# Kernel optimization log

Hardware: AMD Instinct MI355X
Metric: run time of the kernel (lower is better)

Reference implementation:

```python
import jax, jax.numpy as jnp
import numpy as np

N_HEAD = 16
ROPE_BASE = 10000.0


def rope_cos_sin(T, head_dim, dtype):
    inv_freq = 1.0 / (ROPE_BASE ** (jnp.arange(0, head_dim, 2, dtype=jnp.float32) / head_dim))
    t = jnp.arange(T, dtype=jnp.float32)
    freqs = jnp.einsum('i,j->ij', t, inv_freq)          # [T, head_dim/2]
    emb = jnp.concatenate([freqs, freqs], axis=-1)       # [T, head_dim]
    return jnp.cos(emb).astype(dtype), jnp.sin(emb).astype(dtype)


def rotate_half(x):
    h = x.shape[-1] // 2
    return jnp.concatenate([-x[..., h:], x[..., :h]], axis=-1)


def setup_inputs() -> dict:
    key = jax.random.key(0)
    ks = jax.random.split(key, 5)
    B, T, C = 2, 1024, 2048
    s = 0.02
    return {
        'x': jax.random.normal(ks[0], (B, T, C), dtype=jnp.float32),
        'Wq': jax.random.normal(ks[1], (C, C), dtype=jnp.float32) * s,
        'Wk': jax.random.normal(ks[2], (C, C), dtype=jnp.float32) * s,
        'Wv': jax.random.normal(ks[3], (C, C), dtype=jnp.float32) * s,
        'Wo': jax.random.normal(ks[4], (C, C), dtype=jnp.float32) * s,
    }


def reference(x, Wq, Wk, Wv, Wo):
    B, T, C = x.shape
    H = N_HEAD
    D = C // H
    # torch Linear: y = x @ W.T  (W is [out, in])
    q = jnp.einsum('btc,oc->bto', x, Wq).reshape(B, T, H, D).transpose(0, 2, 1, 3)
    k = jnp.einsum('btc,oc->bto', x, Wk).reshape(B, T, H, D).transpose(0, 2, 1, 3)
    v = jnp.einsum('btc,oc->bto', x, Wv).reshape(B, T, H, D).transpose(0, 2, 1, 3)
    cos, sin = rope_cos_sin(T, D, x.dtype)               # [T, D]
    cos = cos[None, None]                                 # [1,1,T,D]
    sin = sin[None, None]
    q = q * cos + rotate_half(q) * sin
    k = k * cos + rotate_half(k) * sin
    scale = 1.0 / jnp.sqrt(jnp.asarray(D, dtype=x.dtype))
    att = jnp.einsum('bhqd,bhkd->bhqk', q, k) * scale    # [B,H,T,T]
    causal = jnp.tril(jnp.ones((T, T), dtype=bool))
    att = jnp.where(causal[None, None], att, jnp.finfo(x.dtype).min)
    att = jax.nn.softmax(att, axis=-1)
    y = jnp.einsum('bhqk,bhkd->bhqd', att, v)            # [B,H,T,D]
    y = y.transpose(0, 2, 1, 3).reshape(B, T, C)
    return jnp.einsum('btc,oc->bto', y, Wo)
```

## Files before the change

kernel.cpp:

```cpp
#include <hip/hip_runtime.h>
#include <stdint.h>

typedef unsigned short u16;
typedef __bf16 bf16x8 __attribute__((ext_vector_type(8)));
typedef float  f32x4  __attribute__((ext_vector_type(4)));

#define B_  2
#define T_  1024
#define C_  2048
#define H_  16
#define D_  128
#define NTENS 4194304

__device__ __forceinline__ u16 f2bf(float f) {
    union { float f; uint32_t u; } v; v.f = f;
    uint32_t r = (v.u + 0x7FFFu + ((v.u >> 16) & 1u)) >> 16;
    return (u16)r;
}
__device__ __forceinline__ float bf2f(u16 h) {
    union { uint32_t u; float f; } v; v.u = ((uint32_t)h) << 16;
    return v.f;
}

__global__ __launch_bounds__(256) void k_convert(
    const float* __restrict__ x, const float* __restrict__ wq,
    const float* __restrict__ wk, const float* __restrict__ wv,
    const float* __restrict__ wo, u16* __restrict__ dst)
{
    int z = blockIdx.z;
    const float* src = (z == 0) ? x : (z == 1) ? wq : (z == 2) ? wk : (z == 3) ? wv : wo;
    u16* d = dst + (size_t)z * NTENS;
    size_t i = ((size_t)blockIdx.x * 256 + threadIdx.x) * 4;
    float4 v = *(const float4*)(src + i);
    ushort4 o;
    o.x = f2bf(v.x); o.y = f2bf(v.y); o.z = f2bf(v.z); o.w = f2bf(v.w);
    *(ushort4*)(d + i) = o;
}

__global__ void k_rope_table(float* __restrict__ ct, float* __restrict__ st)
{
    int t = blockIdx.x, d = threadIdx.x;
    float inv = expf(-(float)d * (9.210340371976184f / 64.0f));
    float th = (float)t * inv;
    float s, c;
    sincosf(th, &s, &c);
    ct[t * 64 + d] = c;
    st[t * 64 + d] = s;
}

template<int MTILE, int EPI>
__device__ __forceinline__ void gemm_tile_nt(
    const u16* __restrict__ A, int lda,
    const u16* __restrict__ Bp, int ldb,
    void* __restrict__ Cp, int ldc,
    int m0, int n0, int K,
    u16* SMEM, const float* __restrict__ ct, const float* __restrict__ st, int z)
{
    constexpr int MF  = MTILE / 16;
    constexpr int ACH = MTILE / 32;
    u16* As = SMEM;
    u16* Bs = SMEM + MTILE * 64;

    const int tid  = threadIdx.x;
    const int wave = tid >> 6;
    const int lane = tid & 63;
    const int wc   = wave << 5;
    const int frow = lane & 15;
    const int quad = lane >> 4;

    const int lrow8  = lane >> 3;
    const int slot   = lane & 7;
    const int gchunk = slot ^ lrow8;

    f32x4 acc[MF][2] = {};

    size_t aoff[ACH], boff[4];
#pragma unroll
    for (int i = 0; i < ACH; ++i) {
        int c = (i << 2) + wave;
        int r = (c << 3) + lrow8;
        aoff[i] = (size_t)(m0 + r) * lda + (gchunk << 3);
    }
#pragma unroll
    for (int i = 0; i < 4; ++i) {
        int r = (i << 5) + (wave << 3) + lrow8;
        boff[i] = (size_t)(n0 + r) * ldb + (gchunk << 3);
    }

    for (int kt = 0; kt < K; kt += 64) {
#pragma unroll
        for (int i = 0; i < ACH; ++i) {
            int c = (i << 2) + wave;
            __builtin_amdgcn_global_load_lds(
                (const __attribute__((address_space(1))) void*)(A + aoff[i] + kt),
                (__attribute__((address_space(3))) void*)(As + (c << 9)), 16, 0, 0);
        }
#pragma unroll
        for (int i = 0; i < 4; ++i) {
            int c = (i << 2) + wave;
            __builtin_amdgcn_global_load_lds(
                (const __attribute__((address_space(1))) void*)(Bp + boff[i] + kt),
                (__attribute__((address_space(3))) void*)(Bs + (c << 9)), 16, 0, 0);
        }
        __syncthreads();

#pragma unroll
        for (int ks = 0; ks < 2; ++ks) {
            int lk = (ks << 2) + quad;
            bf16x8 af[MF], bfv[2];
#pragma unroll
            for (int i = 0; i < MF; ++i) {
                int ar = (i << 4) + frow;
                af[i] = *(const bf16x8*)&As[ar * 64 + ((lk ^ (frow & 7)) << 3)];
            }
#pragma unroll
            for (int j = 0; j < 2; ++j) {
                int br = wc + (j << 4) + frow;
                bfv[j] = *(const bf16x8*)&Bs[br * 64 + ((lk ^ (frow & 7)) << 3)];
            }
#pragma unroll
            for (int i = 0; i < MF; ++i)
#pragma unroll
                for (int j = 0; j < 2; ++j)
                    acc[i][j] = __builtin_amdgcn_mfma_f32_16x16x32_bf16(
                        af[i], bfv[j], acc[i][j], 0, 0, 0);
        }
        __syncthreads();
    }

    if constexpr (EPI == 2) {
        if (z < 2) {
            u16* L = SMEM;
#pragma unroll
            for (int i = 0; i < MF; ++i)
#pragma unroll
                for (int j = 0; j < 2; ++j)
#pragma unroll
                    for (int r = 0; r < 4; ++r) {
                        int rl = (i << 4) + (quad << 2) + r;
                        int d  = wc + (j << 4) + frow;
                        L[rl * 136 + d] = f2bf(acc[i][j][r]);
                    }
            __syncthreads();

            int rl = tid >> 2;
            int d0 = (tid & 3) << 4;
            int t  = (m0 + rl) & 1023;
            uint4 lo4[2], hi4[2];
            lo4[0] = *(const uint4*)&L[rl * 136 + d0];
            lo4[1] = *(const uint4*)&L[rl * 136 + d0 + 8];
            hi4[0] = *(const uint4*)&L[rl * 136 + 64 + d0];
            hi4[1] = *(const uint4*)&L[rl * 136 + 64 + d0 + 8];
            const u16* lo = (const u16*)lo4;
            const u16* hi = (const u16*)hi4;
            float sc = (z == 0) ? 0.08838834764831845f : 1.0f;
            u16 o0[16], o1[16];
            const float* ctp = ct + t * 64 + d0;
            const float* stp = st + t * 64 + d0;
#pragma unroll
            for (int e = 0; e < 16; ++e) {
                float c = ctp[e], s = stp[e];
                float a = bf2f(lo[e]), b = bf2f(hi[e]);
                o0[e] = f2bf((a * c - b * s) * sc);
                o1[e] = f2bf((b * c + a * s) * sc);
            }
            u16* Op = (u16*)Cp;
            size_t rbase = (size_t)(m0 + rl) * ldc + n0;
            *(uint4*)&Op[rbase + d0]          = ((uint4*)o0)[0];
            *(uint4*)&Op[rbase + d0 + 8]      = ((uint4*)o0)[1];
            *(uint4*)&Op[rbase + 64 + d0]     = ((uint4*)o1)[0];
            *(uint4*)&Op[rbase + 64 + d0 + 8] = ((uint4*)o1)[1];
            return;
        }
        u16* Op = (u16*)Cp;
#pragma unroll
        for (int i = 0; i < MF; ++i)
#pragma unroll
            for (int j = 0; j < 2; ++j)
#pragma unroll
                for (int r = 0; r < 4; ++r) {
                    int m = m0 + (i << 4) + (quad << 2) + r;
                    int n = n0 + wc + (j << 4) + frow;
                    Op[(size_t)m * ldc + n] = f2bf(acc[i][j][r]);
                }
        return;
    }

#pragma unroll
    for (int i = 0; i < MF; ++i)
#pragma unroll
        for (int j = 0; j < 2; ++j)
#pragma unroll
            for (int r = 0; r < 4; ++r) {
                int m = m0 + (i << 4) + (quad << 2) + r;
                int n = n0 + wc + (j << 4) + frow;
                if constexpr (EPI == 1)
                    ((u16*)Cp)[(size_t)m * ldc + n] = f2bf(acc[i][j][r]);
                else
                    ((float*)Cp)[(size_t)m * ldc + n] = acc[i][j][r];
            }
}

__global__ __launch_bounds__(256) void k_gemm_qkv(
    const u16* __restrict__ xb, const u16* __restrict__ wq,
    const u16* __restrict__ wk, const u16* __restrict__ wv,
    u16* __restrict__ q, u16* __restrict__ k, u16* __restrict__ v,
    const float* __restrict__ ct, const float* __restrict__ st)
{
    __shared__ u16 SMEM[64 * 64 + 128 * 64];
    int z = blockIdx.z;
    const u16* Bp = (z == 0) ? wq : (z == 1) ? wk : wv;
    u16* Op       = (z == 0) ? q  : (z == 1) ? k  : v;
    gemm_tile_nt<64, 2>(xb, C_, Bp, C_, Op, C_,
                        blockIdx.y * 64, blockIdx.x * 128, C_, SMEM, ct, st, z);
}

__global__ __launch_bounds__(256) void k_flash(
    const u16* __restrict__ qb, const u16* __restrict__ kb,
    const u16* __restrict__ vb, u16* __restrict__ yb)
{
    __shared__ u16 Qs[64 * 128];
    __shared__ u16 Ks[64 * 128];
    __shared__ u16 Vs[128 * 72];

    const int bx  = blockIdx.x;
    const int bh  = bx & 31, b = bh >> 4, h = bh & 15;
    const int qt  = (bx < 256) ? (15 - (bx >> 5)) : ((bx >> 5) - 8);
    const int tid = threadIdx.x, wave = tid >> 6, lane = tid & 63;
    const int frow = lane & 15, quad = lane >> 4;

    const u16* qbase = qb + (size_t)b * (T_ * C_) + h * D_;
    const u16* kbase = kb + (size_t)b * (T_ * C_) + h * D_;
    const u16* vbase = vb + (size_t)b * (T_ * C_) + h * D_;
    const int q0 = qt << 6;

    {
        const int r4 = lane >> 4, s16 = lane & 15;
#pragma unroll
        for (int i = 0; i < 4; ++i) {
            int c = (i << 2) + wave;
            int row = (c << 2) + r4;
            int g = (s16 & 8) | ((s16 & 7) ^ (row & 7));
            __builtin_amdgcn_global_load_lds(
                (const __attribute__((address_space(1))) void*)(qbase + (size_t)(q0 + row) * C_ + (g << 3)),
                (__attribute__((address_space(3))) void*)(Qs + (c << 9)), 16, 0, 0);
        }
    }

    f32x4 Y[8] = {};
    float mrow[4], lrow[4];
#pragma unroll
    for (int r = 0; r < 4; ++r) { mrow[r] = -3e38f; lrow[r] = 0.f; }

    const int tok = q0 + wave * 16 + quad * 4;

    for (int kt = 0; kt <= qt; ++kt) {
        const int k0 = kt << 6;
        {
            const int r4 = lane >> 4, s16 = lane & 15;
#pragma unroll
            for (int i = 0; i < 4; ++i) {
                int c = (i << 2) + wave;
                int row = (c << 2) + r4;
                int g = (s16 & 8) | ((s16 & 7) ^ (row & 7));
                __builtin_amdgcn_global_load_lds(
                    (const __attribute__((address_space(1))) void*)(kbase + (size_t)(k0 + row) * C_ + (g << 3)),
                    (__attribute__((address_space(3))) void*)(Ks + (c << 9)), 16, 0, 0);
            }
        }
        {
#pragma unroll
            for (int i = 0; i < 4; ++i) {
                int idx = (i << 8) + tid;
                int kr = idx & 63;
                int n8 = (idx >> 6) << 3;
                uint4 vv = *(const uint4*)&vbase[(size_t)(k0 + kr) * C_ + n8];
                u16 tmp[8];
                *(uint4*)tmp = vv;
#pragma unroll
                for (int e = 0; e < 8; ++e)
                    Vs[(n8 + e) * 72 + kr] = tmp[e];
            }
        }
        __syncthreads();

        f32x4 S[4] = {};
#pragma unroll
        for (int ks = 0; ks < 4; ++ks) {
            int lk = (ks << 2) + quad;
            int sw = ((lk & 8) | ((lk & 7) ^ (frow & 7))) << 3;
            bf16x8 a = *(const bf16x8*)&Qs[(wave * 16 + frow) * 128 + sw];
#pragma unroll
            for (int jj = 0; jj < 4; ++jj) {
                bf16x8 bb = *(const bf16x8*)&Ks[((jj << 4) + frow) * 128 + sw];
                S[jj] = __builtin_amdgcn_mfma_f32_16x16x32_bf16(a, bb, S[jj], 0, 0, 0);
            }
        }

        if (kt == qt) {
#pragma unroll
            for (int jj = 0; jj < 4; ++jj) {
                int colg = k0 + (jj << 4) + frow;
#pragma unroll
                for (int r = 0; r < 4; ++r)
                    if (colg > tok + r) S[jj][r] = -1e30f;
            }
        }

        float al[4];
#pragma unroll
        for (int r = 0; r < 4; ++r) {
            float tm = fmaxf(fmaxf(S[0][r], S[1][r]), fmaxf(S[2][r], S[3][r]));
#pragma unroll
            for (int off = 8; off > 0; off >>= 1) tm = fmaxf(tm, __shfl_xor(tm, off));
            float mn = fmaxf(mrow[r], tm);
            al[r] = __expf(mrow[r] - mn);
            mrow[r] = mn;
            float rs = 0.f;
#pragma unroll
            for (int jj = 0; jj < 4; ++jj) {
                float e = __expf(S[jj][r] - mn);
                S[jj][r] = e;
                rs += e;
            }
#pragma unroll
            for (int off = 8; off > 0; off >>= 1) rs += __shfl_xor(rs, off);
            lrow[r] = lrow[r] * al[r] + rs;
        }
#pragma unroll
        for (int dj = 0; dj < 8; ++dj)
#pragma unroll
            for (int r = 0; r < 4; ++r) Y[dj][r] *= al[r];

        __syncthreads();

        u16* Ps = Ks;
#pragma unroll
        for (int jj = 0; jj < 4; ++jj)
#pragma unroll
            for (int r = 0; r < 4; ++r)
                Ps[(wave * 16 + quad * 4 + r) * 72 + (jj << 4) + frow] = f2bf(S[jj][r]);

#pragma unroll
        for (int ks = 0; ks < 2; ++ks) {
            bf16x8 pa = *(const bf16x8*)&Ps[(wave * 16 + frow) * 72 + (ks << 5) + (quad << 3)];
#pragma unroll
            for (int dj = 0; dj < 8; ++dj) {
                bf16x8 vv = *(const bf16x8*)&Vs[((dj << 4) + frow) * 72 + (ks << 5) + (quad << 3)];
                Y[dj] = __builtin_amdgcn_mfma_f32_16x16x32_bf16(pa, vv, Y[dj], 0, 0, 0);
            }
        }
        __syncthreads();
    }

    u16* ybase = yb + (size_t)b * (T_ * C_) + h * D_;
#pragma unroll
    for (int r = 0; r < 4; ++r) {
        float inv = 1.0f / lrow[r];
#pragma unroll
        for (int dj = 0; dj < 8; ++dj)
            ybase[(size_t)(tok + r) * C_ + (dj << 4) + frow] = f2bf(Y[dj][r] * inv);
    }
}

__global__ __launch_bounds__(256) void k_gemm_out(
    const u16* __restrict__ yb, const u16* __restrict__ wo, float* __restrict__ out)
{
    __shared__ u16 SMEM[32 * 64 + 128 * 64];
    gemm_tile_nt<32, 0>(yb, C_, wo, C_, out, C_,
                        blockIdx.y * 32, blockIdx.x * 128, C_, SMEM, nullptr, nullptr, 0);
}

extern "C" void kernel_launch(void* const* d_in, const int* in_sizes, int n_in,
                              void* d_out, int out_size, void* d_ws, size_t ws_size,
                              hipStream_t stream)
{
    (void)in_sizes; (void)n_in; (void)out_size; (void)ws_size;
    const float* x  = (const float*)d_in[0];
    const float* Wq = (const float*)d_in[1];
    const float* Wk = (const float*)d_in[2];
    const float* Wv = (const float*)d_in[3];
    const float* Wo = (const float*)d_in[4];

    u16* ws  = (u16*)d_ws;
    u16* xb  = ws;
    u16* wqb = ws + (size_t)1 * NTENS;
    u16* wkb = ws + (size_t)2 * NTENS;
    u16* wvb = ws + (size_t)3 * NTENS;
    u16* wob = ws + (size_t)4 * NTENS;
    u16* qb  = ws + (size_t)5 * NTENS;
    u16* kb  = ws + (size_t)6 * NTENS;
    u16* vb  = ws + (size_t)7 * NTENS;
    u16* yb  = ws + (size_t)8 * NTENS;
    float* ct = (float*)(ws + (size_t)9 * NTENS);
    float* st = ct + 65536;

    k_convert   <<<dim3(4096, 1, 5), 256, 0, stream>>>(x, Wq, Wk, Wv, Wo, ws);
    k_rope_table<<<dim3(1024), 64, 0, stream>>>(ct, st);
    k_gemm_qkv  <<<dim3(16, 32, 3), 256, 0, stream>>>(xb, wqb, wkb, wvb, qb, kb, vb, ct, st);
    k_flash     <<<dim3(512), 256, 0, stream>>>(qb, kb, vb, yb);
    k_gemm_out  <<<dim3(16, 64, 1), 256, 0, stream>>>(yb, wob, (float*)d_out);
}
```

Baseline: 271.3 us.

## Remap GEMM wave columns for register RoPE, widen flash key tile, keep Q in registers

The GEMM wave-to-column mapping changes so each wave holds both halves of a head dimension, letting the RoPE epilogue run in registers without an LDS round trip and barrier. The flash kernel loads Q fragments straight into registers, doubles the key/value tile to 128 rows with a swizzled V layout, and so runs half as many outer iterations. The output GEMM moves to 64-row tiles with half the blocks. These cut LDS traffic, syncs and loop overhead, at the cost of more causal-mask waste on the diagonal tile, more LDS per flash block (lower occupancy), and scattered 2-byte stores in the RoPE epilogue.

New measurement: 262.9 us. 1.03x faster.

```diff
diff --git a/kernel.cpp b/kernel.cpp
--- a/kernel.cpp
+++ b/kernel.cpp
@@ -64,7 +64,6 @@
     const int tid  = threadIdx.x;
     const int wave = tid >> 6;
     const int lane = tid & 63;
-    const int wc   = wave << 5;
     const int frow = lane & 15;
     const int quad = lane >> 4;
 
@@ -115,7 +114,7 @@
             }
 #pragma unroll
             for (int j = 0; j < 2; ++j) {
-                int br = wc + (j << 4) + frow;
+                int br = (wave << 4) + (j << 6) + frow;
                 bfv[j] = *(const bf16x8*)&Bs[br * 64 + ((lk ^ (frow & 7)) << 3)];
             }
 #pragma unroll
@@ -130,60 +129,22 @@
 
     if constexpr (EPI == 2) {
         if (z < 2) {
-            u16* L = SMEM;
+            const int d = (wave << 4) + frow;
+            const float sc = (z == 0) ? 0.08838834764831845f : 1.0f;
+            u16* Op = (u16*)Cp;
 #pragma unroll
             for (int i = 0; i < MF; ++i)
-#pragma unroll
-                for (int j = 0; j < 2; ++j)
-#pragma unroll
-                    for (int r = 0; r < 4; ++r) {
-                        int rl = (i << 4) + (quad << 2) + r;
-                        int d  = wc + (j << 4) + frow;
-                        L[rl * 136 + d] = f2bf(acc[i][j][r]);
-                    }
-            __syncthreads();
-
-            int rl = tid >> 2;
-            int d0 = (tid & 3) << 4;
-            int t  = (m0 + rl) & 1023;
-            uint4 lo4[2], hi4[2];
-            lo4[0] = *(const uint4*)&L[rl * 136 + d0];
-            lo4[1] = *(const uint4*)&L[rl * 136 + d0 + 8];
-            hi4[0] = *(const uint4*)&L[rl * 136 + 64 + d0];
-            hi4[1] = *(const uint4*)&L[rl * 136 + 64 + d0 + 8];
-            const u16* lo = (const u16*)lo4;
-            const u16* hi = (const u16*)hi4;
-            float sc = (z == 0) ? 0.08838834764831845f : 1.0f;
-            u16 o0[16], o1[16];
-            const float* ctp = ct + t * 64 + d0;
-            const float* stp = st + t * 64 + d0;
-#pragma unroll
-            for (int e = 0; e < 16; ++e) {
-                float c = ctp[e], s = stp[e];
-                float a = bf2f(lo[e]), b = bf2f(hi[e]);
-                o0[e] = f2bf((a * c - b * s) * sc);
-                o1[e] = f2bf((b * c + a * s) * sc);
-            }
-            u16* Op = (u16*)Cp;
-            size_t rbase = (size_t)(m0 + rl) * ldc + n0;
-            *(uint4*)&Op[rbase + d0]          = ((uint4*)o0)[0];
-            *(uint4*)&Op[rbase + d0 + 8]      = ((uint4*)o0)[1];
-            *(uint4*)&Op[rbase + 64 + d0]     = ((uint4*)o1)[0];
-            *(uint4*)&Op[rbase + 64 + d0 + 8] = ((uint4*)o1)[1];
-            return;
-        }
-        u16* Op = (u16*)Cp;
-#pragma unroll
-        for (int i = 0; i < MF; ++i)
-#pragma unroll
-            for (int j = 0; j < 2; ++j)
 #pragma unroll
                 for (int r = 0; r < 4; ++r) {
                     int m = m0 + (i << 4) + (quad << 2) + r;
-                    int n = n0 + wc + (j << 4) + frow;
-                    Op[(size_t)m * ldc + n] = f2bf(acc[i][j][r]);
+                    int t = m & 1023;
+                    float c = ct[t * 64 + d], s = st[t * 64 + d];
+                    float a = acc[i][0][r], bb = acc[i][1][r];
+                    Op[(size_t)m * ldc + n0 + d]      = f2bf((a * c - bb * s) * sc);
+                    Op[(size_t)m * ldc + n0 + d + 64] = f2bf((bb * c + a * s) * sc);
                 }
-        return;
+            return;
+        }
     }
 
 #pragma unroll
@@ -193,11 +154,11 @@
 #pragma unroll
             for (int r = 0; r < 4; ++r) {
                 int m = m0 + (i << 4) + (quad << 2) + r;
-                int n = n0 + wc + (j << 4) + frow;
-                if constexpr (EPI == 1)
+                int n = n0 + (wave << 4) + (j << 6) + frow;
+                if constexpr (EPI == 0)
+                    ((float*)Cp)[(size_t)m * ldc + n] = acc[i][j][r];
+                else
                     ((u16*)Cp)[(size_t)m * ldc + n] = f2bf(acc[i][j][r]);
-                else
-                    ((float*)Cp)[(size_t)m * ldc + n] = acc[i][j][r];
             }
 }
 
@@ -219,13 +180,13 @@
     const u16* __restrict__ qb, const u16* __restrict__ kb,
     const u16* __restrict__ vb, u16* __restrict__ yb)
 {
-    __shared__ u16 Qs[64 * 128];
-    __shared__ u16 Ks[64 * 128];
-    __shared__ u16 Vs[128 * 72];
+    __shared__ u16 Ks[128 * 128];
+    __shared__ u16 Vs[128 * 128];
 
     const int bx  = blockIdx.x;
     const int bh  = bx & 31, b = bh >> 4, h = bh & 15;
     const int qt  = (bx < 256) ? (15 - (bx >> 5)) : ((bx >> 5) - 8);
+    const int KT  = (qt >> 1) + 1;
     const int tid = threadIdx.x, wave = tid >> 6, lane = tid & 63;
     const int frow = lane & 15, quad = lane >> 4;
 
@@ -234,32 +195,25 @@
     const u16* vbase = vb + (size_t)b * (T_ * C_) + h * D_;
     const int q0 = qt << 6;
 
-    {
-        const int r4 = lane >> 4, s16 = lane & 15;
-#pragma unroll
-        for (int i = 0; i < 4; ++i) {
-            int c = (i << 2) + wave;
-            int row = (c << 2) + r4;
-            int g = (s16 & 8) | ((s16 & 7) ^ (row & 7));
-            __builtin_amdgcn_global_load_lds(
-                (const __attribute__((address_space(1))) void*)(qbase + (size_t)(q0 + row) * C_ + (g << 3)),
-                (__attribute__((address_space(3))) void*)(Qs + (c << 9)), 16, 0, 0);
-        }
-    }
+    bf16x8 qf[4];
+#pragma unroll
+    for (int ks = 0; ks < 4; ++ks)
+        qf[ks] = *(const bf16x8*)&qbase[(size_t)(q0 + (wave << 4) + frow) * C_
+                                        + (ks << 5) + (quad << 3)];
 
     f32x4 Y[8] = {};
     float mrow[4], lrow[4];
 #pragma unroll
     for (int r = 0; r < 4; ++r) { mrow[r] = -3e38f; lrow[r] = 0.f; }
 
-    const int tok = q0 + wave * 16 + quad * 4;
-
-    for (int kt = 0; kt <= qt; ++kt) {
-        const int k0 = kt << 6;
+    const int tok = q0 + (wave << 4) + (quad << 2);
+
+    for (int kt = 0; kt < KT; ++kt) {
+        const int k0 = kt << 7;
         {
             const int r4 = lane >> 4, s16 = lane & 15;
 #pragma unroll
-            for (int i = 0; i < 4; ++i) {
+            for (int i = 0; i < 8; ++i) {
                 int c = (i << 2) + wave;
                 int row = (c << 2) + r4;
                 int g = (s16 & 8) | ((s16 & 7) ^ (row & 7));
@@ -270,36 +224,39 @@
         }
         {
 #pragma unroll
-            for (int i = 0; i < 4; ++i) {
+            for (int i = 0; i < 8; ++i) {
                 int idx = (i << 8) + tid;
-                int kr = idx & 63;
-                int n8 = (idx >> 6) << 3;
+                int kr  = idx & 127;
+                int n8  = (idx >> 7) << 3;
                 uint4 vv = *(const uint4*)&vbase[(size_t)(k0 + kr) * C_ + n8];
                 u16 tmp[8];
                 *(uint4*)tmp = vv;
-#pragma unroll
-                for (int e = 0; e < 8; ++e)
-                    Vs[(n8 + e) * 72 + kr] = tmp[e];
-            }
-        }
-        __syncthreads();
-
-        f32x4 S[4] = {};
+                int s = kr >> 3, t7 = kr & 7;
+#pragma unroll
+                for (int e = 0; e < 8; ++e) {
+                    int d = n8 + e;
+                    int swz = (s & 8) | ((s & 7) ^ (d & 7));
+                    Vs[d * 128 + (swz << 3) + t7] = tmp[e];
+                }
+            }
+        }
+        __syncthreads();
+
+        f32x4 S[8] = {};
 #pragma unroll
         for (int ks = 0; ks < 4; ++ks) {
             int lk = (ks << 2) + quad;
             int sw = ((lk & 8) | ((lk & 7) ^ (frow & 7))) << 3;
-            bf16x8 a = *(const bf16x8*)&Qs[(wave * 16 + frow) * 128 + sw];
-#pragma unroll
-            for (int jj = 0; jj < 4; ++jj) {
+#pragma unroll
+            for (int jj = 0; jj < 8; ++jj) {
                 bf16x8 bb = *(const bf16x8*)&Ks[((jj << 4) + frow) * 128 + sw];
-                S[jj] = __builtin_amdgcn_mfma_f32_16x16x32_bf16(a, bb, S[jj], 0, 0, 0);
-            }
-        }
-
-        if (kt == qt) {
-#pragma unroll
-            for (int jj = 0; jj < 4; ++jj) {
+                S[jj] = __builtin_amdgcn_mfma_f32_16x16x32_bf16(qf[ks], bb, S[jj], 0, 0, 0);
+            }
+        }
+
+        if (kt == KT - 1) {
+#pragma unroll
+            for (int jj = 0; jj < 8; ++jj) {
                 int colg = k0 + (jj << 4) + frow;
 #pragma unroll
                 for (int r = 0; r < 4; ++r)
@@ -310,7 +267,9 @@
         float al[4];
 #pragma unroll
         for (int r = 0; r < 4; ++r) {
-            float tm = fmaxf(fmaxf(S[0][r], S[1][r]), fmaxf(S[2][r], S[3][r]));
+            float tm = -3e38f;
+#pragma unroll
+            for (int jj = 0; jj < 8; ++jj) tm = fmaxf(tm, S[jj][r]);
 #pragma unroll
             for (int off = 8; off > 0; off >>= 1) tm = fmaxf(tm, __shfl_xor(tm, off));
             float mn = fmaxf(mrow[r], tm);
@@ -318,7 +277,7 @@
             mrow[r] = mn;
             float rs = 0.f;
 #pragma unroll
-            for (int jj = 0; jj < 4; ++jj) {
+            for (int jj = 0; jj < 8; ++jj) {
                 float e = __expf(S[jj][r] - mn);
                 S[jj][r] = e;
                 rs += e;
@@ -336,17 +295,19 @@
 
         u16* Ps = Ks;
 #pragma unroll
-        for (int jj = 0; jj < 4; ++jj)
+        for (int jj = 0; jj < 8; ++jj)
 #pragma unroll
             for (int r = 0; r < 4; ++r)
-                Ps[(wave * 16 + quad * 4 + r) * 72 + (jj << 4) + frow] = f2bf(S[jj][r]);
-
-#pragma unroll
-        for (int ks = 0; ks < 2; ++ks) {
-            bf16x8 pa = *(const bf16x8*)&Ps[(wave * 16 + frow) * 72 + (ks << 5) + (quad << 3)];
+                Ps[((wave << 4) + (quad << 2) + r) * 136 + (jj << 4) + frow] = f2bf(S[jj][r]);
+
+#pragma unroll
+        for (int ks = 0; ks < 4; ++ks) {
+            bf16x8 pa = *(const bf16x8*)&Ps[((wave << 4) + frow) * 136 + (ks << 5) + (quad << 3)];
+            int lk = (ks << 2) + quad;
+            int sw = ((lk & 8) | ((lk & 7) ^ (frow & 7))) << 3;
 #pragma unroll
             for (int dj = 0; dj < 8; ++dj) {
-                bf16x8 vv = *(const bf16x8*)&Vs[((dj << 4) + frow) * 72 + (ks << 5) + (quad << 3)];
+                bf16x8 vv = *(const bf16x8*)&Vs[((dj << 4) + frow) * 128 + sw];
                 Y[dj] = __builtin_amdgcn_mfma_f32_16x16x32_bf16(pa, vv, Y[dj], 0, 0, 0);
             }
         }
@@ -366,9 +327,9 @@
 __global__ __launch_bounds__(256) void k_gemm_out(
     const u16* __restrict__ yb, const u16* __restrict__ wo, float* __restrict__ out)
 {
-    __shared__ u16 SMEM[32 * 64 + 128 * 64];
-    gemm_tile_nt<32, 0>(yb, C_, wo, C_, out, C_,
-                        blockIdx.y * 32, blockIdx.x * 128, C_, SMEM, nullptr, nullptr, 0);
+    __shared__ u16 SMEM[64 * 64 + 128 * 64];
+    gemm_tile_nt<64, 0>(yb, C_, wo, C_, out, C_,
+                        blockIdx.y * 64, blockIdx.x * 128, C_, SMEM, nullptr, nullptr, 0);
 }
 
 extern "C" void kernel_launch(void* const* d_in, const int* in_sizes, int n_in,
@@ -399,5 +360,5 @@
     k_rope_table<<<dim3(1024), 64, 0, stream>>>(ct, st);
     k_gemm_qkv  <<<dim3(16, 32, 3), 256, 0, stream>>>(xb, wqb, wkb, wvb, qb, kb, vb, ct, st);
     k_flash     <<<dim3(512), 256, 0, stream>>>(qb, kb, vb, yb);
-    k_gemm_out  <<<dim3(16, 64, 1), 256, 0, stream>>>(yb, wob, (float*)d_out);
-}
+    k_gemm_out  <<<dim3(16, 32, 1), 256, 0, stream>>>(yb, wob, (float*)d_out);
+}
```
